# Kernel optimization log

Hardware: AMD Instinct MI355X
Metric: run time of the kernel (lower is better)

The kernel has to match this reference:

```python
import jax, jax.numpy as jnp
import numpy as np

B, CIN, COUT = 8, 8, 8
NX, NT = 512, 512
M1, M2 = 4, 4


def setup_inputs() -> dict:
    key = jax.random.key(0)
    k1, k2, k3 = jax.random.split(key, 3)
    scale = 1.0 / (CIN * COUT)
    x = jax.random.normal(k1, (B, CIN, NX, NT), dtype=jnp.float32)
    T = jnp.arange(NT, dtype=jnp.float32).reshape(1, NT)  # time grid
    X = jnp.arange(NX, dtype=jnp.float32).reshape(1, NX)  # space grid
    weights1_ri = scale * jax.random.uniform(k2, (CIN, COUT, M1, M2, 2), dtype=jnp.float32)
    weights2_ri = scale * jax.random.uniform(k3, (CIN, COUT, M1, M2, 2), dtype=jnp.float32)
    return {"x": x, "T": T, "X": X, "weights1_ri": weights1_ri, "weights2_ri": weights2_ri}


def reference(x, T, X, weights1_ri, weights2_ri):
    # subsample every other grid point (as in the torch forward)
    xs = x[:, :, ::2, ::2]                      # [B, Cin, Hs, Ws]
    tx = T[:, ::2]                              # [1, Ws]
    ty = X[:, ::2]                              # [1, Hs]
    dty = ty[0, 1] - ty[0, 0]
    dtx = tx[0, 1] - tx[0, 0]
    Hs, Ws = xs.shape[-2], xs.shape[-1]
    Wr = Ws // 2 + 1

    FW1 = jnp.fft.rfft2(xs)                     # [B, Cin, Hs, Wr] complex64

    two_pi_i = 2.0 * jnp.pi * 1j
    lam1 = (jnp.fft.fftfreq(Hs).astype(jnp.float32) / dty).astype(jnp.complex64) * two_pi_i   # [Hs]
    lam2 = (jnp.fft.rfftfreq(Ws).astype(jnp.float32) / dtx).astype(jnp.complex64) * two_pi_i  # [Wr]

    w1 = (weights1_ri[..., 0] + 1j * weights1_ri[..., 1]).astype(jnp.complex64)
    w2 = (weights2_ri[..., 0] + 1j * weights2_ri[..., 1]).astype(jnp.complex64)

    out2 = jnp.zeros((xs.shape[0], w1.shape[1], Hs, Wr), dtype=jnp.complex64)
    out2 = out2.at[:, :, :M1, :M2].set(
        jnp.einsum('bixy,ioxy->boxy', FW1[:, :, :M1, :M2], w1))
    out2 = out2.at[:, :, -M1:, :M2].set(
        jnp.einsum('bixy,ioxy->boxy', FW1[:, :, -M1:, :M2], w2))

    # inverse transform onto the FULL (non-subsampled) grid via complex exponentials.
    # Same math as the original rank-4 term6 einsum, factorized separably.
    E1 = jnp.exp(lam1[:, None] * X.astype(jnp.complex64).reshape(1, -1))  # [Hs, NX]
    E2 = jnp.exp(lam2[:, None] * T.astype(jnp.complex64).reshape(1, -1))  # [Wr, NT]

    tmp = jnp.einsum('boxw,xz->bozw', out2, E1)   # [B, Cout, NX, Wr]
    x2 = jnp.einsum('bozw,wi->bozi', tmp, E2)     # [B, Cout, NX, NT]
    return jnp.real(x2) / (Ws * Hs)
```

## Files before the change

### kernel.cpp

```cpp
#include <hip/hip_runtime.h>
#include <hip/hip_bf16.h>


#define PI2 6.283185307179586f

__device__ __forceinline__ float foldred(float u, float v, int msk, int lane) {
    float send = (lane & msk) ? u : v;
    float recv = __shfl_xor(send, msk, 64);
    return ((lane & msk) ? v : u) + recv;
}

__global__ __launch_bounds__(512) void k_dft_t(const float* __restrict__ x,
                                               float* __restrict__ Yg) {
    __shared__ float vals[8][64];
    int lane = threadIdx.x & 63;
    int w    = threadIdx.x >> 6;
    int wid  = blockIdx.x * 8 + w;
    int bc = wid >> 8;
    int y  = wid & 255;
    const float2* row2 = (const float2*)(x + ((size_t)bc * 512 + (size_t)(2 * y)) * 512);

    float v[4];
#pragma unroll
    for (int k = 0; k < 4; ++k) v[k] = row2[lane + 64 * k].x;

    float s, c;
    sincosf((PI2 / 256.0f) * (float)lane, &s, &c);
    float pr[4], pim[4];
    pr[0] = 1.f;                         pim[0] = 0.f;
    pr[1] = c;                           pim[1] = -s;
    pr[2] = pr[1]*pr[1] - pim[1]*pim[1]; pim[2] = 2.f*pr[1]*pim[1];
    pr[3] = pr[2]*pr[1] - pim[2]*pim[1]; pim[3] = pr[2]*pim[1] + pim[2]*pr[1];

    float ar[4] = {0.f,0.f,0.f,0.f};
    float ai[4] = {0.f,0.f,0.f,0.f};
#pragma unroll
    for (int k = 0; k < 4; ++k) {
#pragma unroll
        for (int kw = 0; kw < 4; ++kw) {
            int n = (k * kw) & 3;
            float rr, ri;
            if      (n == 0) { rr =  pr[kw];  ri =  pim[kw]; }
            else if (n == 1) { rr =  pim[kw]; ri = -pr[kw];  }
            else if (n == 2) { rr = -pr[kw];  ri = -pim[kw]; }
            else             { rr = -pim[kw]; ri =  pr[kw];  }
            ar[kw] += v[k] * rr;
            ai[kw] += v[k] * ri;
        }
    }
    float A0 = foldred(ar[0], ai[0], 1, lane);
    float A1 = foldred(ar[1], ai[1], 1, lane);
    float A2 = foldred(ar[2], ai[2], 1, lane);
    float A3 = foldred(ar[3], ai[3], 1, lane);
    float B0 = foldred(A0, A1, 2, lane);
    float B1 = foldred(A2, A3, 2, lane);
    float C  = foldred(B0, B1, 4, lane);
    C += __shfl_xor(C, 8, 64);
    C += __shfl_xor(C, 16, 64);
    C += __shfl_xor(C, 32, 64);

    float partner = __shfl_xor(C, 1, 64);
    int midx = lane >> 3;
    float mf = (midx < 4) ? (float)midx : (float)(midx - 8);
    float sn, cs;
    sincosf((PI2 / 256.0f) * mf * (float)y, &sn, &cs);
    float ty  = -sn;
    float sel = (lane & 1) ? ty : -ty;
    vals[w][lane] = C * cs + partner * sel;
    __syncthreads();

    if (threadIdx.x < 64) {
        int b = bc >> 3, ci = bc & 7, g = blockIdx.x & 31;
        float sum = 0.f;
#pragma unroll
        for (int q = 0; q < 8; ++q) sum += vals[q][lane];
        Yg[((size_t)((b * 32 + g) * 8 + ci)) * 64 + lane] = sum;
    }
}

__global__ __launch_bounds__(256) void k_mix_eval(const float* __restrict__ Yg,
                                                  const float* __restrict__ w1,
                                                  const float* __restrict__ w2,
                                                  float* __restrict__ out) {
    __shared__ float vals[4][64];
    __shared__ float lcf[64];

    int lane  = threadIdx.x & 63;
    int w     = threadIdx.x >> 6;
    int bo    = blockIdx.x >> 5;
    int chunk = blockIdx.x & 31;
    int b = bo >> 3, o = bo & 7;

    {
        int midx = lane >> 3, kw = (lane >> 1) & 3, ri = lane & 1, mx = midx & 3;
        const float* wt = (midx < 4) ? w1 : w2;
        float wr_[8], swi_[8];
#pragma unroll
        for (int ci = 0; ci < 8; ++ci) {
            const float* wp = wt + ((((ci * 8 + o) * 4 + mx) * 4 + kw) * 2);
            wr_[ci]  = wp[0];
            swi_[ci] = ri ? wp[1] : -wp[1];
        }
        float acc = 0.f;
#pragma unroll
        for (int gi = 0; gi < 8; ++gi) {
            int g = w + gi * 4;
            const float* Yp = Yg + ((size_t)((b * 32 + g) * 8)) * 64 + lane;
#pragma unroll
            for (int ci = 0; ci < 8; ++ci) {
                float Yv = Yp[ci * 64];
                float pt = __shfl_xor(Yv, 1, 64);
                acc += Yv * wr_[ci] + pt * swi_[ci];
            }
        }
        vals[w][lane] = acc;
    }
    __syncthreads();
    if (w == 0)
        lcf[lane] = vals[0][lane] + vals[1][lane] + vals[2][lane] + vals[3][lane];
    __syncthreads();

    float c1b, s1b;
    sincosf((PI2 / 512.0f) * (float)(lane * 4), &s1b, &c1b);
    const float cr = 0.99992470183839f;
    const float sr = 0.012271538285720f;
    const float inv = 1.0f / 65536.0f;

    int ll = lane & 31;
    int kw = ll & 3, midx = (ll >> 2) & 7;
    float m = (midx < 4) ? (float)midx : (float)(midx - 8);
    float2 cc = make_float2(lcf[ll * 2], lcf[ll * 2 + 1]);
    float sgm = (midx & 1) ? -1.f : 1.f;

#pragma unroll
    for (int e = 0; e < 2; ++e) {
        int z = chunk * 8 + w * 2 + e;

        float ang = (PI2 / 512.0f) * m * (float)z;
        float s, c;
        sincosf(ang, &s, &c);
        float hx = cc.x * c - cc.y * s;
        float hy = cc.x * s + cc.y * c;
        float gx = sgm * hx, gy = sgm * hy;

        float F = foldred(hx, hy, 4, lane);
        F += __shfl_xor(F, 8, 64);
        F += __shfl_xor(F, 16, 64);
        float G = foldred(gx, gy, 4, lane);
        G += __shfl_xor(G, 8, 64);
        G += __shfl_xor(G, 16, 64);
        float h0x = __shfl(F, 0, 64);
        float h1x = __shfl(F, 1, 64), h2x = __shfl(F, 2, 64), h3x = __shfl(F, 3, 64);
        float h1y = __shfl(F, 5, 64), h2y = __shfl(F, 6, 64), h3y = __shfl(F, 7, 64);
        float g0x = __shfl(G, 0, 64);
        float g1x = __shfl(G, 1, 64), g2x = __shfl(G, 2, 64), g3x = __shfl(G, 3, 64);
        float g1y = __shfl(G, 5, 64), g2y = __shfl(G, 6, 64), g3y = __shfl(G, 7, 64);

        float* orow0 = out + (size_t)(bo * 512 + z) * 512;
        float* orow1 = orow0 + 256 * 512;

        float c1 = c1b, s1 = s1b;
        float4 r0, r1, q0, q1;
        float* rp0 = &r0.x; float* rp1 = &r1.x;
        float* qp0 = &q0.x; float* qp1 = &q1.x;
#pragma unroll
        for (int j = 0; j < 4; ++j) {
            float c2a = c1 * c1 - s1 * s1, s2a = 2.f * c1 * s1;
            float c3a = c2a * c1 - s2a * s1, s3a = s2a * c1 + c2a * s1;
            float t1 = h1x * c1  - h1y * s1;
            float t2 = h2x * c2a - h2y * s2a;
            float t3 = h3x * c3a - h3y * s3a;
            rp0[j] = (h0x + t1 + t2 + t3) * inv;
            rp1[j] = (h0x - t1 + t2 - t3) * inv;
            float u1 = g1x * c1  - g1y * s1;
            float u2 = g2x * c2a - g2y * s2a;
            float u3 = g3x * c3a - g3y * s3a;
            qp0[j] = (g0x + u1 + u2 + u3) * inv;
            qp1[j] = (g0x - u1 + u2 - u3) * inv;
            float nc = c1 * cr - s1 * sr;
            float ns = s1 * cr + c1 * sr;
            c1 = nc; s1 = ns;
        }
        *(float4*)(orow0 + lane * 4)       = r0;
        *(float4*)(orow0 + 256 + lane * 4) = r1;
        *(float4*)(orow1 + lane * 4)       = q0;
        *(float4*)(orow1 + 256 + lane * 4) = q1;
    }
}

extern "C" void kernel_launch(void* const* d_in, const int* in_sizes, int n_in,
                              void* d_out, int out_size, void* d_ws, size_t ws_size,
                              hipStream_t stream) {
    const float* x  = (const float*)d_in[0];
    const float* w1 = (const float*)d_in[3];
    const float* w2 = (const float*)d_in[4];
    float* out = (float*)d_out;

    float* Yg = (float*)d_ws;

    k_dft_t<<<2048, 512, 0, stream>>>(x, Yg);
    k_mix_eval<<<2048, 256, 0, stream>>>(Yg, w1, w2, out);
}
```

Baseline: 28.74 us.

## Process two rows per wave in DFT kernel with 128-bit nontemporal loads and stores

Each wave in the forward DFT kernel now handles two subsampled rows. It loads them with 16-byte nontemporal vector loads and folds the four column chunks into an even/odd butterfly before the twiddle multiply. The grid is halved and the partial-sum buffer shrinks from 32 groups to 16, so the mix kernel reads fewer partials. Output stores in the eval kernel become nontemporal to avoid polluting cache. The vector loads still fetch the odd columns that get discarded, so the read traffic is about the same, but there are fewer load instructions per useful element.

```diff
diff --git a/kernel.cpp b/kernel.cpp
--- a/kernel.cpp
+++ b/kernel.cpp
@@ -3,6 +3,8 @@
 
 
 #define PI2 6.283185307179586f
+
+typedef float vfloat4 __attribute__((ext_vector_type(4)));
 
 __device__ __forceinline__ float foldred(float u, float v, int msk, int lane) {
     float send = (lane & msk) ? u : v;
@@ -10,44 +12,7 @@
     return ((lane & msk) ? v : u) + recv;
 }
 
-__global__ __launch_bounds__(512) void k_dft_t(const float* __restrict__ x,
-                                               float* __restrict__ Yg) {
-    __shared__ float vals[8][64];
-    int lane = threadIdx.x & 63;
-    int w    = threadIdx.x >> 6;
-    int wid  = blockIdx.x * 8 + w;
-    int bc = wid >> 8;
-    int y  = wid & 255;
-    const float2* row2 = (const float2*)(x + ((size_t)bc * 512 + (size_t)(2 * y)) * 512);
-
-    float v[4];
-#pragma unroll
-    for (int k = 0; k < 4; ++k) v[k] = row2[lane + 64 * k].x;
-
-    float s, c;
-    sincosf((PI2 / 256.0f) * (float)lane, &s, &c);
-    float pr[4], pim[4];
-    pr[0] = 1.f;                         pim[0] = 0.f;
-    pr[1] = c;                           pim[1] = -s;
-    pr[2] = pr[1]*pr[1] - pim[1]*pim[1]; pim[2] = 2.f*pr[1]*pim[1];
-    pr[3] = pr[2]*pr[1] - pim[2]*pim[1]; pim[3] = pr[2]*pim[1] + pim[2]*pr[1];
-
-    float ar[4] = {0.f,0.f,0.f,0.f};
-    float ai[4] = {0.f,0.f,0.f,0.f};
-#pragma unroll
-    for (int k = 0; k < 4; ++k) {
-#pragma unroll
-        for (int kw = 0; kw < 4; ++kw) {
-            int n = (k * kw) & 3;
-            float rr, ri;
-            if      (n == 0) { rr =  pr[kw];  ri =  pim[kw]; }
-            else if (n == 1) { rr =  pim[kw]; ri = -pr[kw];  }
-            else if (n == 2) { rr = -pr[kw];  ri = -pim[kw]; }
-            else             { rr = -pim[kw]; ri =  pr[kw];  }
-            ar[kw] += v[k] * rr;
-            ai[kw] += v[k] * ri;
-        }
-    }
+__device__ __forceinline__ float fold8(const float* ar, const float* ai, int lane) {
     float A0 = foldred(ar[0], ai[0], 1, lane);
     float A1 = foldred(ar[1], ai[1], 1, lane);
     float A2 = foldred(ar[2], ai[2], 1, lane);
@@ -58,23 +23,77 @@
     C += __shfl_xor(C, 8, 64);
     C += __shfl_xor(C, 16, 64);
     C += __shfl_xor(C, 32, 64);
-
-    float partner = __shfl_xor(C, 1, 64);
+    return C;
+}
+
+__global__ __launch_bounds__(512) void k_dft_t(const float* __restrict__ x,
+                                               float* __restrict__ Yg) {
+    __shared__ float vals[8][64];
+    int lane = threadIdx.x & 63;
+    int w    = threadIdx.x >> 6;
+    int bc   = blockIdx.x >> 4;
+    int g    = blockIdx.x & 15;
+    int y0   = 2 * (g * 8 + w);
+
+    const vfloat4* r0 = (const vfloat4*)(x + ((size_t)bc * 512 + (size_t)(2 * y0)) * 512);
+    const vfloat4* r1 = (const vfloat4*)(x + ((size_t)bc * 512 + (size_t)(2 * y0 + 2)) * 512);
+    vfloat4 a0 = __builtin_nontemporal_load(&r0[lane]);
+    vfloat4 a1 = __builtin_nontemporal_load(&r0[lane + 64]);
+    vfloat4 b0 = __builtin_nontemporal_load(&r1[lane]);
+    vfloat4 b1 = __builtin_nontemporal_load(&r1[lane + 64]);
+
+    float s, c;
+    sincosf((PI2 / 128.0f) * (float)lane, &s, &c);
+    float er[4], ei[4], orE[4], oiE[4];
+    er[0] = 1.f; ei[0] = 0.f;
+    er[1] = c;   ei[1] = -s;
+    er[2] = er[1]*er[1] - ei[1]*ei[1];  ei[2] = 2.f*er[1]*ei[1];
+    er[3] = er[2]*er[1] - ei[2]*ei[1];  ei[3] = er[2]*ei[1] + ei[2]*er[1];
+    const float rr1 = 0.999698818696204f, ri1 = -0.024541228522912f;
+    const float rr2 = 0.998795456205172f, ri2 = -0.049067674327418f;
+    const float rr3 = 0.997290456678690f, ri3 = -0.073564563599667f;
+    orE[0] = 1.f; oiE[0] = 0.f;
+    orE[1] = er[1]*rr1 - ei[1]*ri1;  oiE[1] = er[1]*ri1 + ei[1]*rr1;
+    orE[2] = er[2]*rr2 - ei[2]*ri2;  oiE[2] = er[2]*ri2 + ei[2]*rr2;
+    orE[3] = er[3]*rr3 - ei[3]*ri3;  oiE[3] = er[3]*ri3 + ei[3]*rr3;
+
+    float arA[4], aiA[4], arB[4], aiB[4];
+#pragma unroll
+    for (int kw = 0; kw < 4; ++kw) {
+        float sgn = (kw & 1) ? -1.f : 1.f;
+        float eA = a0[0] + sgn * a1[0], oA = a0[2] + sgn * a1[2];
+        float eB = b0[0] + sgn * b1[0], oB = b0[2] + sgn * b1[2];
+        arA[kw] = eA * er[kw] + oA * orE[kw];
+        aiA[kw] = eA * ei[kw] + oA * oiE[kw];
+        arB[kw] = eB * er[kw] + oB * orE[kw];
+        aiB[kw] = eB * ei[kw] + oB * oiE[kw];
+    }
+    float Ca = fold8(arA, aiA, lane);
+    float Cb = fold8(arB, aiB, lane);
+
     int midx = lane >> 3;
     float mf = (midx < 4) ? (float)midx : (float)(midx - 8);
-    float sn, cs;
-    sincosf((PI2 / 256.0f) * mf * (float)y, &sn, &cs);
-    float ty  = -sn;
-    float sel = (lane & 1) ? ty : -ty;
-    vals[w][lane] = C * cs + partner * sel;
+    float snm, csm;
+    sincosf((PI2 / 256.0f) * mf * (float)y0, &snm, &csm);
+    float ty0 = -snm;
+    float smm, cmm;
+    sincosf((PI2 / 256.0f) * mf, &smm, &cmm);
+    float cs1 = csm * cmm + ty0 * smm;
+    float ty1 = ty0 * cmm - csm * smm;
+
+    float pa = __shfl_xor(Ca, 1, 64);
+    float pb = __shfl_xor(Cb, 1, 64);
+    float selA = (lane & 1) ? ty0 : -ty0;
+    float selB = (lane & 1) ? ty1 : -ty1;
+    vals[w][lane] = Ca * csm + pa * selA + Cb * cs1 + pb * selB;
     __syncthreads();
 
     if (threadIdx.x < 64) {
-        int b = bc >> 3, ci = bc & 7, g = blockIdx.x & 31;
+        int b = bc >> 3, ci = bc & 7;
         float sum = 0.f;
 #pragma unroll
         for (int q = 0; q < 8; ++q) sum += vals[q][lane];
-        Yg[((size_t)((b * 32 + g) * 8 + ci)) * 64 + lane] = sum;
+        Yg[((size_t)((b * 16 + g) * 8 + ci)) * 64 + lane] = sum;
     }
 }
 
@@ -103,9 +122,9 @@
         }
         float acc = 0.f;
 #pragma unroll
-        for (int gi = 0; gi < 8; ++gi) {
+        for (int gi = 0; gi < 4; ++gi) {
             int g = w + gi * 4;
-            const float* Yp = Yg + ((size_t)((b * 32 + g) * 8)) * 64 + lane;
+            const float* Yp = Yg + ((size_t)((b * 16 + g) * 8)) * 64 + lane;
 #pragma unroll
             for (int ci = 0; ci < 8; ++ci) {
                 float Yv = Yp[ci * 64];
@@ -160,9 +179,7 @@
         float* orow1 = orow0 + 256 * 512;
 
         float c1 = c1b, s1 = s1b;
-        float4 r0, r1, q0, q1;
-        float* rp0 = &r0.x; float* rp1 = &r1.x;
-        float* qp0 = &q0.x; float* qp1 = &q1.x;
+        vfloat4 r0, r1, q0, q1;
 #pragma unroll
         for (int j = 0; j < 4; ++j) {
             float c2a = c1 * c1 - s1 * s1, s2a = 2.f * c1 * s1;
@@ -170,21 +187,21 @@
             float t1 = h1x * c1  - h1y * s1;
             float t2 = h2x * c2a - h2y * s2a;
             float t3 = h3x * c3a - h3y * s3a;
-            rp0[j] = (h0x + t1 + t2 + t3) * inv;
-            rp1[j] = (h0x - t1 + t2 - t3) * inv;
+            r0[j] = (h0x + t1 + t2 + t3) * inv;
+            r1[j] = (h0x - t1 + t2 - t3) * inv;
             float u1 = g1x * c1  - g1y * s1;
             float u2 = g2x * c2a - g2y * s2a;
             float u3 = g3x * c3a - g3y * s3a;
-            qp0[j] = (g0x + u1 + u2 + u3) * inv;
-            qp1[j] = (g0x - u1 + u2 - u3) * inv;
+            q0[j] = (g0x + u1 + u2 + u3) * inv;
+            q1[j] = (g0x - u1 + u2 - u3) * inv;
             float nc = c1 * cr - s1 * sr;
             float ns = s1 * cr + c1 * sr;
             c1 = nc; s1 = ns;
         }
-        *(float4*)(orow0 + lane * 4)       = r0;
-        *(float4*)(orow0 + 256 + lane * 4) = r1;
-        *(float4*)(orow1 + lane * 4)       = q0;
-        *(float4*)(orow1 + 256 + lane * 4) = q1;
+        __builtin_nontemporal_store(r0, (vfloat4*)(orow0 + lane * 4));
+        __builtin_nontemporal_store(r1, (vfloat4*)(orow0 + 256 + lane * 4));
+        __builtin_nontemporal_store(q0, (vfloat4*)(orow1 + lane * 4));
+        __builtin_nontemporal_store(q1, (vfloat4*)(orow1 + 256 + lane * 4));
     }
 }
 
@@ -198,6 +215,6 @@
 
     float* Yg = (float*)d_ws;
 
-    k_dft_t<<<2048, 512, 0, stream>>>(x, Yg);
+    k_dft_t<<<1024, 512, 0, stream>>>(x, Yg);
     k_mix_eval<<<2048, 256, 0, stream>>>(Yg, w1, w2, out);
 }
```

Measured after the change: 25.48 us. 1.13x faster.
